# Optimization experiments

Hardware: AMD Instinct MI355X
Metric: run time of the kernel (lower is better)

Reference implementation:

```python
import jax, jax.numpy as jnp
import numpy as np

IMG = 224   # img_size
K = 8       # num_bands
E = 256     # embed_dim


def _radial_masks(size, k):
    # Faithful to torch _create_radial_masks: center = size//2, max_r = size/sqrt(2)
    center = size // 2
    y, x = jnp.meshgrid(jnp.arange(size), jnp.arange(size), indexing='ij')
    r = jnp.sqrt(((x - center) ** 2 + (y - center) ** 2).astype(jnp.float32))
    max_r = size / np.sqrt(2.0)
    step = np.float32(max_r / k)
    i = jnp.arange(k, dtype=jnp.float32)[:, None, None]
    masks = ((r[None] >= step * i) & (r[None] < step * (i + 1.0))).astype(jnp.float32)
    return masks  # [K, H, W]


def setup_inputs() -> dict:
    key = jax.random.key(0)
    ks = jax.random.split(key, 3)
    x = jax.random.normal(ks[0], (64, 3, IMG, IMG), dtype=jnp.float32)
    W1 = jax.random.normal(ks[1], (3, E), dtype=jnp.float32) * 0.3
    b1 = jnp.zeros((E,), jnp.float32)
    gamma = jnp.ones((E,), jnp.float32)
    beta = jnp.zeros((E,), jnp.float32)
    W2 = jax.random.normal(ks[2], (E, E), dtype=jnp.float32) * (1.0 / np.sqrt(E))
    b2 = jnp.zeros((E,), jnp.float32)
    return {"x": x, "W1": W1, "b1": b1, "gamma": gamma, "beta": beta, "W2": W2, "b2": b2}


def reference(x, W1, b1, gamma, beta, W2, b2):
    masks = _radial_masks(IMG, K)                    # [K,H,W], binary, non-overlapping
    x_gray = x.mean(axis=1)                          # [B,H,W]
    fft = jnp.fft.fftshift(jnp.fft.fft2(x_gray), axes=(-2, -1))
    mag = jnp.log1p(jnp.abs(fft))                    # log(1+|F|)
    mu = mag.mean(axis=(1, 2), keepdims=True)
    sd = jnp.std(mag, axis=(1, 2), keepdims=True, ddof=1) + 1e-6  # torch .std is unbiased
    magn = (mag - mu) / sd                           # [B,H,W]

    msum = masks.sum(axis=(1, 2))                    # [K], true mask pixel counts
    mask_sums = msum + 1e-6
    s1 = jnp.einsum('bhw,khw->bk', magn, masks)      # per-band sum
    s2 = jnp.einsum('bhw,khw->bk', magn * magn, masks)
    means = s1 / mask_sums
    # sum((magn - means)^2 * mask) = s2 - 2*means*s1 + means^2 * msum  (exact expansion)
    var_num = s2 - 2.0 * means * s1 + (means ** 2) * msum
    stds = jnp.sqrt(var_num / mask_sums + 1e-6)
    # masked_fill(mask==0, -1e9) then amax over H,W
    maxs = jnp.max(jnp.where(masks[None] > 0, magn[:, None], -1e9), axis=(2, 3))

    feats = jnp.stack([means, stds, maxs], axis=-1)  # [B,K,3]
    h = feats @ W1 + b1                              # [B,K,E]
    hm = h.mean(axis=-1, keepdims=True)
    hv = h.var(axis=-1, keepdims=True)
    h = (h - hm) / jnp.sqrt(hv + 1e-5) * gamma + beta  # LayerNorm, eps=1e-5
    h = jax.nn.relu(h)
    return h @ W2 + b2                               # [B,K,E]
```

## Files before the change

### kernel.cpp

```cpp
#include <hip/hip_runtime.h>
#include <math.h>

#define IMG 224
#define NPIX 50176
#define BATCH 64
#define EDIM 256

typedef _Float16 f16;
typedef __attribute__((ext_vector_type(8))) _Float16 f16x8;
typedef __attribute__((ext_vector_type(4))) _Float16 f16x4;
typedef __attribute__((ext_vector_type(4))) float f32x4;
typedef unsigned int u32;


#define GLD16(gp, lp)                                                          \
  __builtin_amdgcn_global_load_lds(                                            \
      (const __attribute__((address_space(1))) u32*)(gp),                      \
      (__attribute__((address_space(3))) u32*)(lp), 16, 0, 0)

__global__ __launch_bounds__(256) void gemmA_kernel(const float* __restrict__ x,
                                                    f16* __restrict__ B2t,
                                                    float* __restrict__ stats) {
  __shared__ float T[224];
  __shared__ f16 As[2][64][64];
  __shared__ f16 Bs[2][256][64];
  int m0 = blockIdx.x * 64;
  int tid = threadIdx.x;
  int lane = tid & 63, wid = tid >> 6;
  int wr = wid >> 1, wc = wid & 1;

  if (blockIdx.x == 0) {
#pragma unroll
    for (int i = 0; i < 9; ++i) {
      int idx = i * 256 + tid;
      if (idx < BATCH * 34) stats[idx] = 0.f;
    }
  }

  int arow = tid >> 2;
  int aseg = tid & 3;
  int am = m0 + arow;
  int ab = am / 224, ah = am - ab * 224;
  const float* px = x + (size_t)ab * 3 * NPIX + ah * IMG;
  int s0 = (aseg * 2) ^ (arow & 7);
  int s1 = (aseg * 2 + 1) ^ (arow & 7);

  f32x4 xl[3][4];
  f32x4 acc[2][8];
#pragma unroll
  for (int i = 0; i < 2; ++i)
#pragma unroll
    for (int j = 0; j < 8; ++j) acc[i][j] = (f32x4){0.f, 0.f, 0.f, 0.f};

  auto issueA = [&](int t) {
    int kb = t * 64 + aseg * 16;
    if (kb < 224) {
#pragma unroll
      for (int c = 0; c < 3; ++c)
#pragma unroll
        for (int q = 0; q < 4; ++q)
          xl[c][q] = *(const f32x4*)(px + c * NPIX + kb + q * 4);
    }
  };
  auto writeA = [&](int bufi, int t) {
    int kb = t * 64 + aseg * 16;
    f16x8 h0, h1;
    if (kb < 224) {
#pragma unroll
      for (int j = 0; j < 8; ++j) {
        int q = j >> 2, r = j & 3;
        h0[j] = (f16)((xl[0][q][r] + xl[1][q][r] + xl[2][q][r]) * (1.0f / 3.0f));
      }
#pragma unroll
      for (int j = 0; j < 8; ++j) {
        int q = 2 + (j >> 2), r = j & 3;
        h1[j] = (f16)((xl[0][q][r] + xl[1][q][r] + xl[2][q][r]) * (1.0f / 3.0f));
      }
    } else {
#pragma unroll
      for (int j = 0; j < 8; ++j) { h0[j] = (f16)0.f; h1[j] = (f16)0.f; }
    }
    *(f16x8*)&As[bufi][arow][s0 * 8] = h0;
    *(f16x8*)&As[bufi][arow][s1 * 8] = h1;
  };
  auto computeB = [&](int bufi, int t) {
    int row = tid;
    int v = (row < 113) ? row : row - 113;
    u32 off = (row < 113) ? 0u : 56u;
    u32 idx = ((u32)(t * 64) * (u32)v + off) % 224u;
#pragma unroll
    for (int g = 0; g < 8; ++g) {
      f16x8 hv;
#pragma unroll
      for (int j = 0; j < 8; ++j) {
        hv[j] = (f16)T[idx];
        idx += v; if (idx >= 224u) idx -= 224u;
      }
      *(f16x8*)&Bs[bufi][row][(g ^ (row & 7)) * 8] = hv;
    }
  };

  issueA(0);
  if (tid < 224) T[tid] = cospif((float)tid / 112.0f);
  __syncthreads();
  computeB(0, 0);

#pragma unroll 1
  for (int t = 0; t < 4; ++t) {
    int cur = t & 1;
    asm volatile("s_waitcnt vmcnt(0)" ::: "memory");
    writeA(cur, t);
    asm volatile("s_waitcnt lgkmcnt(0)" ::: "memory");
    __builtin_amdgcn_s_barrier();
    if (t < 3) { issueA(t + 1); computeB(cur ^ 1, t + 1); }
#pragma unroll
    for (int kk = 0; kk < 2; ++kk) {
      f16x8 af[2], bfr[8];
#pragma unroll
      for (int mi = 0; mi < 2; ++mi) {
        int row = wr * 32 + mi * 16 + (lane & 15);
        int slot = (kk * 4 + (lane >> 4)) ^ (row & 7);
        af[mi] = *(const f16x8*)&As[cur][row][slot * 8];
      }
#pragma unroll
      for (int nj = 0; nj < 8; ++nj) {
        int row = wc * 128 + nj * 16 + (lane & 15);
        int slot = (kk * 4 + (lane >> 4)) ^ (row & 7);
        bfr[nj] = *(const f16x8*)&Bs[cur][row][slot * 8];
      }
#pragma unroll
      for (int mi = 0; mi < 2; ++mi)
#pragma unroll
        for (int nj = 0; nj < 8; ++nj)
          acc[mi][nj] = __builtin_amdgcn_mfma_f32_16x16x32_f16(
              af[mi], bfr[nj], acc[mi][nj], 0, 0, 0);
    }
    __builtin_amdgcn_s_barrier();
  }

  int mbase = m0 + wr * 32, nbase = wc * 128;
#pragma unroll
  for (int mi = 0; mi < 2; ++mi) {
#pragma unroll
    for (int nj = 0; nj < 8; ++nj) {
      int c = nbase + nj * 16 + (lane & 15);
      if (c >= 226) continue;
      int m = mbase + mi * 16 + ((lane >> 4) << 2);
      int b = m / 224;
      int h = m - b * 224;
      int v = c, kb = h;
      if (c >= 113) { v = c - 113; kb = 224 + h; }
      size_t off = (size_t)(b * 128 + v) * 448 + kb;
      f32x4 y = acc[mi][nj];
      f16x4 hv;
#pragma unroll
      for (int r = 0; r < 4; ++r) hv[r] = (f16)y[r];
      *(f16x4*)&B2t[off] = hv;
    }
  }
}

__global__ __launch_bounds__(256) void gemmB_kernel(const f16* __restrict__ B2t,
                                                    float* __restrict__ stats) {
  __shared__ float T[224];
  __shared__ f16 As[2][64][64];
  __shared__ f16 Bs[3][128][64];
  int tid = threadIdx.x;
  int lane = tid & 63, wid = tid >> 6;
  int wr = wid >> 1, wc = wid & 1;

  int bid = blockIdx.x;
  int nb = (bid & 7) * 56 + (bid >> 3);
  int b = nb / 7;
  int m0 = (nb - b * 7) * 64;
  const f16* Bb = B2t + (size_t)b * 128 * 448;

  int srow = lane >> 3;
  int sk8 = (lane & 7) ^ srow;

  f32x4 acc[2][4];
#pragma unroll
  for (int i = 0; i < 2; ++i)
#pragma unroll
    for (int j = 0; j < 4; ++j) acc[i][j] = (f32x4){0.f, 0.f, 0.f, 0.f};

  auto issueB = [&](int t) {
    int k0 = t * 64;
    int bi = t % 3;
#pragma unroll
    for (int ci = 0; ci < 4; ++ci) {
      int j = wid * 4 + ci;
      GLD16(Bb + (size_t)(j * 8 + srow) * 448 + k0 + sk8 * 8,
            &Bs[bi][0][0] + j * 512);
    }
  };
  auto computeA = [&](int bufi, int t) {
    int row = tid >> 2, seg = tid & 3;
    int rr = m0 + row;
    u32 u = (u32)(rr >> 1);
    int imrow = rr & 1;
    int kb = t * 64 + seg * 16;
    int kim = kb >= 224;
    u32 kq = (u32)(kb - (kim ? 224 : 0));
    u32 off = imrow ? (kim ? 0u : 56u) : (kim ? 168u : 0u);
    u32 idx = (u * kq + off) % 224u;
#pragma unroll
    for (int g = 0; g < 2; ++g) {
      f16x8 hv;
#pragma unroll
      for (int j = 0; j < 8; ++j) {
        hv[j] = (f16)T[idx];
        idx += u; if (idx >= 224u) idx -= 224u;
      }
      int lg = seg * 2 + g;
      *(f16x8*)&As[bufi][row][(lg ^ (row & 7)) * 8] = hv;
    }
  };

  if (tid < 224) T[tid] = cospif((float)tid / 112.0f);
  issueB(0);
  issueB(1);
  __syncthreads();
  computeA(0, 0);

#pragma unroll 1
  for (int t = 0; t < 7; ++t) {
    int cur = t & 1;
    if (t < 6) {
      asm volatile("s_waitcnt vmcnt(4)" ::: "memory");
    } else {
      asm volatile("s_waitcnt vmcnt(0)" ::: "memory");
    }
    asm volatile("s_waitcnt lgkmcnt(0)" ::: "memory");
    __builtin_amdgcn_s_barrier();
    if (t + 2 <= 6) issueB(t + 2);
    if (t < 6) computeA(cur ^ 1, t + 1);
    int bcur = t % 3;
#pragma unroll
    for (int kk = 0; kk < 2; ++kk) {
      f16x8 af[2], bfr[4];
#pragma unroll
      for (int mi = 0; mi < 2; ++mi) {
        int row = wr * 32 + mi * 16 + (lane & 15);
        int slot = (kk * 4 + (lane >> 4)) ^ (row & 7);
        af[mi] = *(const f16x8*)&As[cur][row][slot * 8];
      }
#pragma unroll
      for (int nj = 0; nj < 4; ++nj) {
        int row = wc * 64 + nj * 16 + (lane & 15);
        int slot = (kk * 4 + (lane >> 4)) ^ (row & 7);
        bfr[nj] = *(const f16x8*)&Bs[bcur][row][slot * 8];
      }
#pragma unroll
      for (int mi = 0; mi < 2; ++mi)
#pragma unroll
        for (int nj = 0; nj < 4; ++nj)
          acc[mi][nj] = __builtin_amdgcn_mfma_f32_16x16x32_f16(
              af[mi], bfr[nj], acc[mi][nj], 0, 0, 0);
    }
    __builtin_amdgcn_s_barrier();
  }

  int rbase = m0 + wr * 32;
  const float step = (float)(158.39191898578665 / 8.0);
  float gsum = 0.f, gsq = 0.f;
  float s1[8] = {0}, s2[8] = {0}, cnt[8] = {0};
  float mx[8] = {0, 0, 0, 0, 0, 0, 0, 0};

#pragma unroll
  for (int mi = 0; mi < 2; ++mi) {
#pragma unroll
    for (int nj = 0; nj < 4; ++nj) {
      int n = wc * 64 + nj * 16 + (lane & 15);
      if (n >= 113) continue;
      float wgt = (n >= 1 && n <= 111) ? 2.f : 1.f;
      float dx2 = (float)(n * n);
      int rr = rbase + mi * 16 + ((lane >> 4) << 2);
      f32x4 f = acc[mi][nj];
#pragma unroll
      for (int p = 0; p < 2; ++p) {
        int u = (rr >> 1) + p;
        float re = f[2 * p], im = f[2 * p + 1];
        float mv = log1pf(sqrtf(re * re + im * im));
        int a = (u <= 111) ? u : 224 - u;
        float r = sqrtf((float)(a * a) + dx2);
        int bd = 255;
#pragma unroll
        for (int k = 0; k < 8; k++) {
          float lo = step * (float)k;
          float hi = step * (float)(k + 1);
          if (r >= lo && r < hi) bd = k;
        }
        float wm = wgt * mv;
        gsum += wm;
        gsq += wm * mv;
#pragma unroll
        for (int k = 0; k < 8; k++) {
          bool m = (bd == k);
          s1[k] += m ? wm : 0.f;
          s2[k] += m ? wm * mv : 0.f;
          cnt[k] += m ? wgt : 0.f;
          mx[k] = m ? fmaxf(mx[k], mv) : mx[k];
        }
      }
    }
  }

  float vals[34];
  vals[0] = gsum; vals[1] = gsq;
#pragma unroll
  for (int k = 0; k < 8; k++) {
    vals[2 + k] = s1[k]; vals[10 + k] = s2[k]; vals[18 + k] = mx[k]; vals[26 + k] = cnt[k];
  }
#pragma unroll
  for (int i = 0; i < 34; i++) {
    float v = vals[i];
    const bool isMax = (i >= 18 && i < 26);
#pragma unroll
    for (int off = 32; off > 0; off >>= 1) {
      float o = __shfl_down(v, off);
      v = isMax ? fmaxf(v, o) : (v + o);
    }
    vals[i] = v;
  }
  float* red = (float*)&As[0][0][0];
  if ((tid & 63) == 0) {
#pragma unroll
    for (int i = 0; i < 34; i++) red[wid * 34 + i] = vals[i];
  }
  __syncthreads();
  if (tid < 34) {
    bool isMax = (tid >= 18 && tid < 26);
    float v = red[tid];
#pragma unroll
    for (int ww = 1; ww < 4; ww++) {
      float o = red[ww * 34 + tid];
      v = isMax ? fmaxf(v, o) : (v + o);
    }
    if (isMax)
      atomicMax((u32*)&stats[b * 34 + tid], __float_as_uint(v));
    else
      atomicAdd(&stats[b * 34 + tid], v);
  }
}

__global__ __launch_bounds__(256) void mlp_kernel(const float* __restrict__ stats,
                                                  const float* __restrict__ W1,
                                                  const float* __restrict__ b1,
                                                  const float* __restrict__ gamma,
                                                  const float* __restrict__ beta,
                                                  const float* __restrict__ W2m,
                                                  const float* __restrict__ b2,
                                                  float* __restrict__ out) {
  int bk = blockIdx.x;
  int b = bk >> 3, k = bk & 7;
  int e = threadIdx.x;

  __shared__ float st[34];
  if (e < 34) st[e] = stats[b * 34 + e];
  __syncthreads();

  const float N = (float)NPIX;
  float mu = st[0] / N;
  float varg = fmaxf(st[1] - N * mu * mu, 0.0f) / (N - 1.0f);
  float sd = sqrtf(varg) + 1e-6f;

  float s1r = st[2 + k], s2r = st[10 + k], mxr = st[18 + k], cntk = st[26 + k];
  float ms = cntk + 1e-6f;
  float s1n = (s1r - mu * cntk) / sd;
  float s2n = (s2r - 2.0f * mu * s1r + mu * mu * cntk) / (sd * sd);
  float mean_k = s1n / ms;
  float var_num = s2n - 2.0f * mean_k * s1n + mean_k * mean_k * cntk;
  float std_k = sqrtf(var_num / ms + 1e-6f);
  float max_k = (mxr - mu) / sd;

  float h = mean_k * W1[e] + std_k * W1[EDIM + e] + max_k * W1[2 * EDIM + e] + b1[e];

  float s = h, q = h * h;
#pragma unroll
  for (int off = 32; off > 0; off >>= 1) {
    s += __shfl_down(s, off);
    q += __shfl_down(q, off);
  }
  __shared__ float rs[4], rq[4];
  __shared__ float hmS, hvS;
  if ((e & 63) == 0) { rs[e >> 6] = s; rq[e >> 6] = q; }
  __syncthreads();
  if (e == 0) {
    float ts = rs[0] + rs[1] + rs[2] + rs[3];
    float tq = rq[0] + rq[1] + rq[2] + rq[3];
    float hm = ts / 256.0f;
    hmS = hm;
    hvS = fmaxf(tq / 256.0f - hm * hm, 0.0f);
  }
  __syncthreads();
  float hn = (h - hmS) / sqrtf(hvS + 1e-5f) * gamma[e] + beta[e];
  float hr = fmaxf(hn, 0.0f);

  __shared__ float hs[EDIM];
  hs[e] = hr;
  __syncthreads();

  float acc = b2[e];
#pragma unroll 8
  for (int j = 0; j < EDIM; j++) acc += hs[j] * W2m[j * EDIM + e];
  out[(size_t)bk * EDIM + e] = acc;
}

extern "C" void kernel_launch(void* const* d_in, const int* in_sizes, int n_in,
                              void* d_out, int out_size, void* d_ws, size_t ws_size,
                              hipStream_t stream) {
  const float* x     = (const float*)d_in[0];
  const float* W1    = (const float*)d_in[1];
  const float* b1    = (const float*)d_in[2];
  const float* gamma = (const float*)d_in[3];
  const float* beta  = (const float*)d_in[4];
  const float* W2m   = (const float*)d_in[5];
  const float* b2    = (const float*)d_in[6];
  float* out = (float*)d_out;

  char* W = (char*)d_ws;
  f16* B2t = (f16*)W;
  float* stats = (float*)(W + 7340032);

  gemmA_kernel<<<dim3(224), dim3(256), 0, stream>>>(x, B2t, stats);
  gemmB_kernel<<<dim3(448), dim3(256), 0, stream>>>(B2t, stats);
  mlp_kernel<<<dim3(BATCH * 8), dim3(256), 0, stream>>>(stats, W1, b1, gamma, beta, W2m, b2, out);
}
```

Before: 54.84 us.

## Halve gemmA row tile, generate DFT twiddles by recurrence, batch two bands per MLP block

gemmA now uses 32-row tiles with each wave owning a 64-column slice, so it launches twice as many blocks (448) to fill more CUs. Both GEMM kernels stop doing modular-index LDS table lookups for cosine twiddles and generate them with the Chebyshev recurrence cos((n+1)x)=2cos(x)cos(nx)-cos((n-1)x), which removes LDS reads and index arithmetic. Because the recurrence runs in fp32 for up to 64 steps, rounding error can build up compared with exact table values. The MLP kernel now handles two bands per block, so each W2 load is reused twice and half as many blocks are launched.

```diff
diff --git a/kernel.cpp b/kernel.cpp
--- a/kernel.cpp
+++ b/kernel.cpp
@@ -22,12 +22,11 @@
                                                     f16* __restrict__ B2t,
                                                     float* __restrict__ stats) {
   __shared__ float T[224];
-  __shared__ f16 As[2][64][64];
+  __shared__ f16 As[2][32][64];
   __shared__ f16 Bs[2][256][64];
-  int m0 = blockIdx.x * 64;
+  int m0 = blockIdx.x * 32;
   int tid = threadIdx.x;
   int lane = tid & 63, wid = tid >> 6;
-  int wr = wid >> 1, wc = wid & 1;
 
   if (blockIdx.x == 0) {
 #pragma unroll
@@ -37,64 +36,62 @@
     }
   }
 
-  int arow = tid >> 2;
-  int aseg = tid & 3;
+  int arow = tid >> 3;
+  int aseg = tid & 7;
   int am = m0 + arow;
   int ab = am / 224, ah = am - ab * 224;
   const float* px = x + (size_t)ab * 3 * NPIX + ah * IMG;
-  int s0 = (aseg * 2) ^ (arow & 7);
-  int s1 = (aseg * 2 + 1) ^ (arow & 7);
-
-  f32x4 xl[3][4];
-  f32x4 acc[2][8];
+  int s0 = aseg ^ (arow & 7);
+
+  f32x4 xl[3][2];
+  f32x4 acc[2][4];
 #pragma unroll
   for (int i = 0; i < 2; ++i)
 #pragma unroll
-    for (int j = 0; j < 8; ++j) acc[i][j] = (f32x4){0.f, 0.f, 0.f, 0.f};
+    for (int j = 0; j < 4; ++j) acc[i][j] = (f32x4){0.f, 0.f, 0.f, 0.f};
 
   auto issueA = [&](int t) {
-    int kb = t * 64 + aseg * 16;
+    int kb = t * 64 + aseg * 8;
     if (kb < 224) {
 #pragma unroll
-      for (int c = 0; c < 3; ++c)
-#pragma unroll
-        for (int q = 0; q < 4; ++q)
-          xl[c][q] = *(const f32x4*)(px + c * NPIX + kb + q * 4);
+      for (int c = 0; c < 3; ++c) {
+        xl[c][0] = *(const f32x4*)(px + c * NPIX + kb);
+        xl[c][1] = *(const f32x4*)(px + c * NPIX + kb + 4);
+      }
     }
   };
   auto writeA = [&](int bufi, int t) {
-    int kb = t * 64 + aseg * 16;
-    f16x8 h0, h1;
+    int kb = t * 64 + aseg * 8;
+    f16x8 h0;
     if (kb < 224) {
 #pragma unroll
       for (int j = 0; j < 8; ++j) {
         int q = j >> 2, r = j & 3;
         h0[j] = (f16)((xl[0][q][r] + xl[1][q][r] + xl[2][q][r]) * (1.0f / 3.0f));
       }
-#pragma unroll
-      for (int j = 0; j < 8; ++j) {
-        int q = 2 + (j >> 2), r = j & 3;
-        h1[j] = (f16)((xl[0][q][r] + xl[1][q][r] + xl[2][q][r]) * (1.0f / 3.0f));
-      }
     } else {
 #pragma unroll
-      for (int j = 0; j < 8; ++j) { h0[j] = (f16)0.f; h1[j] = (f16)0.f; }
+      for (int j = 0; j < 8; ++j) h0[j] = (f16)0.f;
     }
     *(f16x8*)&As[bufi][arow][s0 * 8] = h0;
-    *(f16x8*)&As[bufi][arow][s1 * 8] = h1;
   };
   auto computeB = [&](int bufi, int t) {
     int row = tid;
     int v = (row < 113) ? row : row - 113;
     u32 off = (row < 113) ? 0u : 56u;
-    u32 idx = ((u32)(t * 64) * (u32)v + off) % 224u;
+    u32 idx0 = ((u32)(t * 64) * (u32)v + off) % 224u;
+    u32 idxm = (idx0 >= (u32)v) ? idx0 - (u32)v : idx0 + 224u - (u32)v;
+    float cur = T[idx0];
+    float prev = T[idxm];
+    float k2c = 2.0f * T[v];
 #pragma unroll
     for (int g = 0; g < 8; ++g) {
       f16x8 hv;
 #pragma unroll
       for (int j = 0; j < 8; ++j) {
-        hv[j] = (f16)T[idx];
-        idx += v; if (idx >= 224u) idx -= 224u;
+        hv[j] = (f16)cur;
+        float nxt = __builtin_fmaf(k2c, cur, -prev);
+        prev = cur; cur = nxt;
       }
       *(f16x8*)&Bs[bufi][row][(g ^ (row & 7)) * 8] = hv;
     }
@@ -115,37 +112,37 @@
     if (t < 3) { issueA(t + 1); computeB(cur ^ 1, t + 1); }
 #pragma unroll
     for (int kk = 0; kk < 2; ++kk) {
-      f16x8 af[2], bfr[8];
+      f16x8 af[2], bfr[4];
 #pragma unroll
       for (int mi = 0; mi < 2; ++mi) {
-        int row = wr * 32 + mi * 16 + (lane & 15);
+        int row = mi * 16 + (lane & 15);
         int slot = (kk * 4 + (lane >> 4)) ^ (row & 7);
         af[mi] = *(const f16x8*)&As[cur][row][slot * 8];
       }
 #pragma unroll
-      for (int nj = 0; nj < 8; ++nj) {
-        int row = wc * 128 + nj * 16 + (lane & 15);
+      for (int nj = 0; nj < 4; ++nj) {
+        int row = wid * 64 + nj * 16 + (lane & 15);
         int slot = (kk * 4 + (lane >> 4)) ^ (row & 7);
         bfr[nj] = *(const f16x8*)&Bs[cur][row][slot * 8];
       }
 #pragma unroll
       for (int mi = 0; mi < 2; ++mi)
 #pragma unroll
-        for (int nj = 0; nj < 8; ++nj)
+        for (int nj = 0; nj < 4; ++nj)
           acc[mi][nj] = __builtin_amdgcn_mfma_f32_16x16x32_f16(
               af[mi], bfr[nj], acc[mi][nj], 0, 0, 0);
     }
     __builtin_amdgcn_s_barrier();
   }
 
-  int mbase = m0 + wr * 32, nbase = wc * 128;
+  int nbase = wid * 64;
 #pragma unroll
   for (int mi = 0; mi < 2; ++mi) {
 #pragma unroll
-    for (int nj = 0; nj < 8; ++nj) {
+    for (int nj = 0; nj < 4; ++nj) {
       int c = nbase + nj * 16 + (lane & 15);
       if (c >= 226) continue;
-      int m = mbase + mi * 16 + ((lane >> 4) << 2);
+      int m = m0 + mi * 16 + ((lane >> 4) << 2);
       int b = m / 224;
       int h = m - b * 224;
       int v = c, kb = h;
@@ -203,17 +200,21 @@
     int kim = kb >= 224;
     u32 kq = (u32)(kb - (kim ? 224 : 0));
     u32 off = imrow ? (kim ? 0u : 56u) : (kim ? 168u : 0u);
-    u32 idx = (u * kq + off) % 224u;
+    u32 idx0 = (u * kq + off) % 224u;
+    u32 idxm = (idx0 >= u) ? idx0 - u : idx0 + 224u - u;
+    float cur = T[idx0];
+    float prev = T[idxm];
+    float k2c = 2.0f * T[u];
 #pragma unroll
     for (int g = 0; g < 2; ++g) {
       f16x8 hv;
 #pragma unroll
       for (int j = 0; j < 8; ++j) {
-        hv[j] = (f16)T[idx];
-        idx += u; if (idx >= 224u) idx -= 224u;
-      }
-      int lg = seg * 2 + g;
-      *(f16x8*)&As[bufi][row][(lg ^ (row & 7)) * 8] = hv;
+        hv[j] = (f16)cur;
+        float nxt = __builtin_fmaf(k2c, cur, -prev);
+        prev = cur; cur = nxt;
+      }
+      *(f16x8*)&As[bufi][row][((seg * 2 + g) ^ (row & 7)) * 8] = hv;
     }
   };
 
@@ -352,9 +353,11 @@
                                                   const float* __restrict__ W2m,
                                                   const float* __restrict__ b2,
                                                   float* __restrict__ out) {
-  int bk = blockIdx.x;
-  int b = bk >> 3, k = bk & 7;
+  int blk = blockIdx.x;
+  int b = blk >> 2;
+  int k0 = (blk & 3) * 2;
   int e = threadIdx.x;
+  int lane = e & 63, wave = e >> 6;
 
   __shared__ float st[34];
   if (e < 34) st[e] = stats[b * 34 + e];
@@ -365,46 +368,69 @@
   float varg = fmaxf(st[1] - N * mu * mu, 0.0f) / (N - 1.0f);
   float sd = sqrtf(varg) + 1e-6f;
 
-  float s1r = st[2 + k], s2r = st[10 + k], mxr = st[18 + k], cntk = st[26 + k];
-  float ms = cntk + 1e-6f;
-  float s1n = (s1r - mu * cntk) / sd;
-  float s2n = (s2r - 2.0f * mu * s1r + mu * mu * cntk) / (sd * sd);
-  float mean_k = s1n / ms;
-  float var_num = s2n - 2.0f * mean_k * s1n + mean_k * mean_k * cntk;
-  float std_k = sqrtf(var_num / ms + 1e-6f);
-  float max_k = (mxr - mu) / sd;
-
-  float h = mean_k * W1[e] + std_k * W1[EDIM + e] + max_k * W1[2 * EDIM + e] + b1[e];
-
-  float s = h, q = h * h;
-#pragma unroll
-  for (int off = 32; off > 0; off >>= 1) {
-    s += __shfl_down(s, off);
-    q += __shfl_down(q, off);
-  }
-  __shared__ float rs[4], rq[4];
-  __shared__ float hmS, hvS;
-  if ((e & 63) == 0) { rs[e >> 6] = s; rq[e >> 6] = q; }
+  float g_e = gamma[e], bt_e = beta[e], b1_e = b1[e];
+  float w1a = W1[e], w1b = W1[EDIM + e], w1c = W1[2 * EDIM + e];
+
+  float h[2];
+#pragma unroll
+  for (int q = 0; q < 2; ++q) {
+    int k = k0 + q;
+    float s1r = st[2 + k], s2r = st[10 + k], mxr = st[18 + k], cntk = st[26 + k];
+    float ms = cntk + 1e-6f;
+    float s1n = (s1r - mu * cntk) / sd;
+    float s2n = (s2r - 2.0f * mu * s1r + mu * mu * cntk) / (sd * sd);
+    float mean_k = s1n / ms;
+    float var_num = s2n - 2.0f * mean_k * s1n + mean_k * mean_k * cntk;
+    float std_k = sqrtf(var_num / ms + 1e-6f);
+    float max_k = (mxr - mu) / sd;
+    h[q] = mean_k * w1a + std_k * w1b + max_k * w1c + b1_e;
+  }
+
+  float v4[4] = {h[0], h[0] * h[0], h[1], h[1] * h[1]};
+#pragma unroll
+  for (int i = 0; i < 4; ++i) {
+#pragma unroll
+    for (int off = 32; off > 0; off >>= 1) v4[i] += __shfl_down(v4[i], off);
+  }
+  __shared__ float red[4][4];
+  __shared__ float mm[4];
+  if (lane == 0) {
+#pragma unroll
+    for (int i = 0; i < 4; ++i) red[wave][i] = v4[i];
+  }
   __syncthreads();
   if (e == 0) {
-    float ts = rs[0] + rs[1] + rs[2] + rs[3];
-    float tq = rq[0] + rq[1] + rq[2] + rq[3];
-    float hm = ts / 256.0f;
-    hmS = hm;
-    hvS = fmaxf(tq / 256.0f - hm * hm, 0.0f);
-  }
-  __syncthreads();
-  float hn = (h - hmS) / sqrtf(hvS + 1e-5f) * gamma[e] + beta[e];
-  float hr = fmaxf(hn, 0.0f);
-
-  __shared__ float hs[EDIM];
-  hs[e] = hr;
-  __syncthreads();
-
-  float acc = b2[e];
+#pragma unroll
+    for (int i = 0; i < 4; ++i) {
+      float t = red[0][i] + red[1][i] + red[2][i] + red[3][i];
+      red[0][i] = t;
+    }
+    float hm0 = red[0][0] / 256.0f, hm1 = red[0][2] / 256.0f;
+    mm[0] = hm0;
+    mm[1] = fmaxf(red[0][1] / 256.0f - hm0 * hm0, 0.0f);
+    mm[2] = hm1;
+    mm[3] = fmaxf(red[0][3] / 256.0f - hm1 * hm1, 0.0f);
+  }
+  __syncthreads();
+
+  __shared__ float hsT[EDIM][2];
+#pragma unroll
+  for (int q = 0; q < 2; ++q) {
+    float hn = (h[q] - mm[2 * q]) / sqrtf(mm[2 * q + 1] + 1e-5f) * g_e + bt_e;
+    hsT[e][q] = fmaxf(hn, 0.0f);
+  }
+  __syncthreads();
+
+  float a0 = b2[e], a1 = a0;
 #pragma unroll 8
-  for (int j = 0; j < EDIM; j++) acc += hs[j] * W2m[j * EDIM + e];
-  out[(size_t)bk * EDIM + e] = acc;
+  for (int j = 0; j < EDIM; j++) {
+    float w = W2m[j * EDIM + e];
+    float2 hp = *(const float2*)&hsT[j][0];
+    a0 += hp.x * w;
+    a1 += hp.y * w;
+  }
+  out[(size_t)(b * 8 + k0) * EDIM + e] = a0;
+  out[(size_t)(b * 8 + k0 + 1) * EDIM + e] = a1;
 }
 
 extern "C" void kernel_launch(void* const* d_in, const int* in_sizes, int n_in,
@@ -423,7 +449,7 @@
   f16* B2t = (f16*)W;
   float* stats = (float*)(W + 7340032);
 
-  gemmA_kernel<<<dim3(224), dim3(256), 0, stream>>>(x, B2t, stats);
+  gemmA_kernel<<<dim3(448), dim3(256), 0, stream>>>(x, B2t, stats);
   gemmB_kernel<<<dim3(448), dim3(256), 0, stream>>>(B2t, stats);
-  mlp_kernel<<<dim3(BATCH * 8), dim3(256), 0, stream>>>(stats, W1, b1, gamma, beta, W2m, b2, out);
+  mlp_kernel<<<dim3(256), dim3(256), 0, stream>>>(stats, W1, b1, gamma, beta, W2m, b2, out);
 }
```

After: 49.89 us. 1.1x faster.
